# Performance work log

Measured on AMD Instinct MI355X. Metric: run time of the kernel, lower is better.

Reference implementation:

```python
import jax, jax.numpy as jnp
import numpy as np

BZ, C, H, W, M = 8, 64, 64, 64, 2048  # N = H*W = 4096 scene-graph nodes


def setup_inputs() -> dict:
    key = jax.random.key(0)
    k1, k2 = jax.random.split(key)
    sg_node_feats = jax.random.normal(k1, (BZ, C, H, W), dtype=jnp.float32)
    # weighted adjacency from SG nodes (N) to KG nodes (M)
    sg_kg_adj = jax.random.uniform(k2, (BZ, H * W, M), dtype=jnp.float32)
    return {"sg_node_feats": sg_node_feats, "sg_kg_adj": sg_kg_adj}


def reference(sg_node_feats, sg_kg_adj):
    bz, channels, height, width = sg_node_feats.shape
    x = sg_node_feats.reshape(bz, channels, height * width)  # (bz, C, N)
    degrees = sg_kg_adj.sum(axis=1)                          # (bz, M)
    norm = jnp.maximum(degrees, 1.0)                         # (bz, M)
    # broadcast-multiply + sum over N == batched GEMM (bz,C,N) x (bz,N,M)
    out = jnp.einsum('bcn,bnm->bcm', x, sg_kg_adj) / norm[:, None, :]
    return out.transpose(0, 2, 1)                            # (bz, M, C)
```

## Files before the change

### kernel.cpp

```cpp
#include <hip/hip_runtime.h>


typedef short bf16x8 __attribute__((ext_vector_type(8)));
typedef float f32x4 __attribute__((ext_vector_type(4)));

#define BZc 8
#define Cc 64
#define Nc 4096
#define Mc 2048
#define BMc 64
#define BKc 64
#define KITERS (Nc / BKc)
#define SDW 36

__device__ __forceinline__ unsigned int pkbf(float a, float b) {
  unsigned int ua = __float_as_uint(a) + 0x8000u;
  unsigned int ub = __float_as_uint(b) + 0x8000u;
  return (ua >> 16) | (ub & 0xffff0000u);
}

__global__ __launch_bounds__(512) void sgkg_kernel(
    const float* __restrict__ x,
    const float* __restrict__ adj,
    float* __restrict__ out)
{
  __shared__ unsigned int adjT[BMc * SDW];
  __shared__ float degs[BMc];

  const int t = threadIdx.x;
  const int l = t & 63;
  const int w = t >> 6;

  const int bz     = blockIdx.x >> 5;
  const int m_base = (blockIdx.x & 31) * BMc;

  const int mg  = ((w & 1) << 3) | (l & 7);
  const int p   = ((w >> 1) << 3) | (l >> 3);
  const int sm0 = mg << 2;

  const float* aptr =
      adj + (size_t)bz * Nc * Mc + (size_t)(2 * p) * Mc + (m_base + sm0);
  const int wb = SDW * sm0 + ((((p >> 2) ^ (mg & 7))) << 2) + (p & 3);

  const int m_off = (w & 1) << 5;
  const int c_b   = (w >> 1) << 4;
  const int l15   = l & 15;
  const int l4    = l >> 4;

  const float* xb =
      x + ((size_t)bz * Cc + (c_b + l15)) * Nc + (l4 << 3);

  int aaddr[2][2];
#pragma unroll
  for (int tm = 0; tm < 2; ++tm) {
    const int m  = m_off + tm * 16 + l15;
    const int pi = (m >> 2) & 7;
    aaddr[tm][0] = SDW * m + (((l4) ^ pi) << 2);
    aaddr[tm][1] = SDW * m + (((4 + l4) ^ pi) << 2);
  }

  if (t < BMc) degs[t] = 0.0f;

  f32x4 acc0 = {0.f, 0.f, 0.f, 0.f};
  f32x4 acc1 = {0.f, 0.f, 0.f, 0.f};
  float dacc0 = 0.f, dacc1 = 0.f, dacc2 = 0.f, dacc3 = 0.f;

  float4 r0 = *(const float4*)aptr;
  float4 r1 = *(const float4*)(aptr + Mc);

  for (int it = 0; it < KITERS; ++it) {
    __syncthreads();

    adjT[wb          ] = pkbf(r0.x, r1.x);
    adjT[wb +     SDW] = pkbf(r0.y, r1.y);
    adjT[wb + 2 * SDW] = pkbf(r0.z, r1.z);
    adjT[wb + 3 * SDW] = pkbf(r0.w, r1.w);

    dacc0 += r0.x + r1.x;
    dacc1 += r0.y + r1.y;
    dacc2 += r0.z + r1.z;
    dacc3 += r0.w + r1.w;

    const float* anext = (it + 1 < KITERS) ? (aptr + (size_t)BKc * Mc) : aptr;
    float4 s0 = *(const float4*)anext;
    float4 s1 = *(const float4*)(anext + Mc);

    const float* xit = xb + it * BKc;
    float4 blo0 = *(const float4*)(xit);
    float4 bhi0 = *(const float4*)(xit + 4);
    float4 blo1 = *(const float4*)(xit + 32);
    float4 bhi1 = *(const float4*)(xit + 36);
    union { uint4 u; bf16x8 v; } B0, B1;
    B0.u = make_uint4(pkbf(blo0.x, blo0.y), pkbf(blo0.z, blo0.w),
                      pkbf(bhi0.x, bhi0.y), pkbf(bhi0.z, bhi0.w));
    B1.u = make_uint4(pkbf(blo1.x, blo1.y), pkbf(blo1.z, blo1.w),
                      pkbf(bhi1.x, bhi1.y), pkbf(bhi1.z, bhi1.w));

    __syncthreads();

    bf16x8 a00 = *(const bf16x8*)(adjT + aaddr[0][0]);
    bf16x8 a10 = *(const bf16x8*)(adjT + aaddr[1][0]);
    acc0 = __builtin_amdgcn_mfma_f32_16x16x32_bf16(a00, B0.v, acc0, 0, 0, 0);
    acc1 = __builtin_amdgcn_mfma_f32_16x16x32_bf16(a10, B0.v, acc1, 0, 0, 0);
    bf16x8 a01 = *(const bf16x8*)(adjT + aaddr[0][1]);
    bf16x8 a11 = *(const bf16x8*)(adjT + aaddr[1][1]);
    acc0 = __builtin_amdgcn_mfma_f32_16x16x32_bf16(a01, B1.v, acc0, 0, 0, 0);
    acc1 = __builtin_amdgcn_mfma_f32_16x16x32_bf16(a11, B1.v, acc1, 0, 0, 0);

    aptr = anext;
    r0 = s0;
    r1 = s1;
  }

  __syncthreads();
  atomicAdd(&degs[sm0 + 0], dacc0);
  atomicAdd(&degs[sm0 + 1], dacc1);
  atomicAdd(&degs[sm0 + 2], dacc2);
  atomicAdd(&degs[sm0 + 3], dacc3);
  __syncthreads();

#pragma unroll
  for (int tm = 0; tm < 2; ++tm) {
    const f32x4 acc = tm ? acc1 : acc0;
#pragma unroll
    for (int r = 0; r < 4; ++r) {
      const int ml    = m_off + tm * 16 + (l4 << 2) + r;
      const float nrm = fmaxf(degs[ml], 1.0f);
      const float v   = acc[r] / nrm;
      const size_t o  = ((size_t)(bz * Mc + m_base + ml)) * Cc + (c_b + l15);
      out[o] = v;
    }
  }
}

extern "C" void kernel_launch(void* const* d_in, const int* in_sizes, int n_in,
                              void* d_out, int out_size, void* d_ws, size_t ws_size,
                              hipStream_t stream) {
  const float* x   = (const float*)d_in[0];
  const float* adj = (const float*)d_in[1];
  float* out       = (float*)d_out;
  (void)in_sizes; (void)n_in; (void)out_size; (void)d_ws; (void)ws_size;

  sgkg_kernel<<<dim3(BZc * (Mc / BMc)), dim3(512), 0, stream>>>(x, adj, out);
}
```

Measured before the change: 378.9 us.

## Split N reduction across two blocks and add a normalization pass

```diff
diff --git a/kernel.cpp b/kernel.cpp
--- a/kernel.cpp
+++ b/kernel.cpp
@@ -10,8 +10,13 @@
 #define Mc 2048
 #define BMc 64
 #define BKc 64
-#define KITERS (Nc / BKc)
+#define NSPLIT 2
+#define NHALF (Nc / NSPLIT)
+#define KITERS (NHALF / BKc)
 #define SDW 36
+
+#define PSUM_ELEMS (BZc * Mc * Cc)
+#define PDEG_ELEMS (BZc * Mc)
 
 __device__ __forceinline__ unsigned int pkbf(float a, float b) {
   unsigned int ua = __float_as_uint(a) + 0x8000u;
@@ -19,10 +24,10 @@
   return (ua >> 16) | (ub & 0xffff0000u);
 }
 
-__global__ __launch_bounds__(512) void sgkg_kernel(
+__global__ __launch_bounds__(512, 4) void sgkg_kernel(
     const float* __restrict__ x,
     const float* __restrict__ adj,
-    float* __restrict__ out)
+    float* __restrict__ ws)
 {
   __shared__ unsigned int adjT[BMc * SDW];
   __shared__ float degs[BMc];
@@ -31,15 +36,16 @@
   const int l = t & 63;
   const int w = t >> 6;
 
-  const int bz     = blockIdx.x >> 5;
-  const int m_base = (blockIdx.x & 31) * BMc;
+  const int bz     = blockIdx.x >> 6;
+  const int m_base = ((blockIdx.x >> 1) & 31) * BMc;
+  const int kh     = blockIdx.x & 1;
 
   const int mg  = ((w & 1) << 3) | (l & 7);
   const int p   = ((w >> 1) << 3) | (l >> 3);
   const int sm0 = mg << 2;
 
   const float* aptr =
-      adj + (size_t)bz * Nc * Mc + (size_t)(2 * p) * Mc + (m_base + sm0);
+      adj + (size_t)bz * Nc * Mc + (size_t)(kh * NHALF + 2 * p) * Mc + (m_base + sm0);
   const int wb = SDW * sm0 + ((((p >> 2) ^ (mg & 7))) << 2) + (p & 3);
 
   const int m_off = (w & 1) << 5;
@@ -48,7 +54,7 @@
   const int l4    = l >> 4;
 
   const float* xb =
-      x + ((size_t)bz * Cc + (c_b + l15)) * Nc + (l4 << 3);
+      x + ((size_t)bz * Cc + (c_b + l15)) * Nc + kh * NHALF + (l4 << 3);
 
   int aaddr[2][2];
 #pragma unroll
@@ -67,6 +73,10 @@
 
   float4 r0 = *(const float4*)aptr;
   float4 r1 = *(const float4*)(aptr + Mc);
+  float4 xr0 = *(const float4*)(xb);
+  float4 xr1 = *(const float4*)(xb + 4);
+  float4 xr2 = *(const float4*)(xb + 32);
+  float4 xr3 = *(const float4*)(xb + 36);
 
   for (int it = 0; it < KITERS; ++it) {
     __syncthreads();
@@ -85,16 +95,17 @@
     float4 s0 = *(const float4*)anext;
     float4 s1 = *(const float4*)(anext + Mc);
 
-    const float* xit = xb + it * BKc;
-    float4 blo0 = *(const float4*)(xit);
-    float4 bhi0 = *(const float4*)(xit + 4);
-    float4 blo1 = *(const float4*)(xit + 32);
-    float4 bhi1 = *(const float4*)(xit + 36);
+    const float* xnp = (it + 1 < KITERS) ? (xb + (it + 1) * BKc) : xb;
+    float4 y0 = *(const float4*)(xnp);
+    float4 y1 = *(const float4*)(xnp + 4);
+    float4 y2 = *(const float4*)(xnp + 32);
+    float4 y3 = *(const float4*)(xnp + 36);
+
     union { uint4 u; bf16x8 v; } B0, B1;
-    B0.u = make_uint4(pkbf(blo0.x, blo0.y), pkbf(blo0.z, blo0.w),
-                      pkbf(bhi0.x, bhi0.y), pkbf(bhi0.z, bhi0.w));
-    B1.u = make_uint4(pkbf(blo1.x, blo1.y), pkbf(blo1.z, blo1.w),
-                      pkbf(bhi1.x, bhi1.y), pkbf(bhi1.z, bhi1.w));
+    B0.u = make_uint4(pkbf(xr0.x, xr0.y), pkbf(xr0.z, xr0.w),
+                      pkbf(xr1.x, xr1.y), pkbf(xr1.z, xr1.w));
+    B1.u = make_uint4(pkbf(xr2.x, xr2.y), pkbf(xr2.z, xr2.w),
+                      pkbf(xr3.x, xr3.y), pkbf(xr3.z, xr3.w));
 
     __syncthreads();
 
@@ -108,8 +119,8 @@
     acc1 = __builtin_amdgcn_mfma_f32_16x16x32_bf16(a11, B1.v, acc1, 0, 0, 0);
 
     aptr = anext;
-    r0 = s0;
-    r1 = s1;
+    r0 = s0; r1 = s1;
+    xr0 = y0; xr1 = y1; xr2 = y2; xr3 = y3;
   }
 
   __syncthreads();
@@ -117,20 +128,46 @@
   atomicAdd(&degs[sm0 + 1], dacc1);
   atomicAdd(&degs[sm0 + 2], dacc2);
   atomicAdd(&degs[sm0 + 3], dacc3);
-  __syncthreads();
 
+  float* psum = ws + (size_t)kh * PSUM_ELEMS;
 #pragma unroll
   for (int tm = 0; tm < 2; ++tm) {
     const f32x4 acc = tm ? acc1 : acc0;
 #pragma unroll
     for (int r = 0; r < 4; ++r) {
-      const int ml    = m_off + tm * 16 + (l4 << 2) + r;
-      const float nrm = fmaxf(degs[ml], 1.0f);
-      const float v   = acc[r] / nrm;
-      const size_t o  = ((size_t)(bz * Mc + m_base + ml)) * Cc + (c_b + l15);
-      out[o] = v;
+      const int ml   = m_off + tm * 16 + (l4 << 2) + r;
+      const size_t o = ((size_t)(bz * Mc + m_base + ml)) * Cc + (c_b + l15);
+      psum[o] = acc[r];
     }
   }
+
+  __syncthreads();
+  if (t < BMc) {
+    float* pdeg = ws + 2 * (size_t)PSUM_ELEMS + (size_t)kh * PDEG_ELEMS;
+    pdeg[bz * Mc + m_base + t] = degs[t];
+  }
+}
+
+__global__ __launch_bounds__(256) void norm_kernel(
+    const float* __restrict__ ws, float* __restrict__ out)
+{
+  const int i = blockIdx.x * 256 + threadIdx.x;
+  const float4* p0 = (const float4*)ws;
+  const float4* p1 = (const float4*)(ws + PSUM_ELEMS);
+  const float* d0  = ws + 2 * (size_t)PSUM_ELEMS;
+  const float* d1  = d0 + PDEG_ELEMS;
+
+  const int bm = i >> 4;
+  const float den = fmaxf(d0[bm] + d1[bm], 1.0f);
+
+  float4 a = p0[i];
+  float4 b = p1[i];
+  float4 r;
+  r.x = (a.x + b.x) / den;
+  r.y = (a.y + b.y) / den;
+  r.z = (a.z + b.z) / den;
+  r.w = (a.w + b.w) / den;
+  ((float4*)out)[i] = r;
 }
 
 extern "C" void kernel_launch(void* const* d_in, const int* in_sizes, int n_in,
@@ -139,7 +176,9 @@
   const float* x   = (const float*)d_in[0];
   const float* adj = (const float*)d_in[1];
   float* out       = (float*)d_out;
-  (void)in_sizes; (void)n_in; (void)out_size; (void)d_ws; (void)ws_size;
+  float* ws        = (float*)d_ws;
+  (void)in_sizes; (void)n_in; (void)out_size; (void)ws_size;
 
-  sgkg_kernel<<<dim3(BZc * (Mc / BMc)), dim3(512), 0, stream>>>(x, adj, out);
+  sgkg_kernel<<<dim3(BZc * (Mc / BMc) * NSPLIT), dim3(512), 0, stream>>>(x, adj, ws);
+  norm_kernel<<<dim3(PSUM_ELEMS / 4 / 256), dim3(256), 0, stream>>>(ws, out);
 }
```

Result: no change. 384.9 us (+1.6%).
